# Kernel tuning notes

Measured on AMD Instinct MI355X. Metric: run time of the kernel, lower is better.

The kernel has to match this reference:

```python
import jax, jax.numpy as jnp
import numpy as np

B, T, D, H = 32, 2048, 256, 256  # batch, length, input_size, hidden_size


def _lstm_layer(x, W_ih, W_hh, b, reverse):
    """Single-direction LSTM over time. x: [B,T,Din]; W_ih: [4H,Din]; W_hh: [4H,H]; b: [4H].
    Gate order: i, f, g, o (PyTorch convention). Returns hidden states [B,T,H]."""
    # Precompute input contribution for all timesteps in one big GEMM.
    xg = jnp.einsum('btd,gd->btg', x, W_ih) + b  # [B,T,4H]
    Hh = W_hh.shape[1]
    Bb = x.shape[0]

    def step(carry, xg_t):
        h, c = carry
        g = xg_t + h @ W_hh.T  # [B,4H]
        i, f, gc, o = jnp.split(g, 4, axis=-1)
        c = jax.nn.sigmoid(f) * c + jax.nn.sigmoid(i) * jnp.tanh(gc)
        h = jax.nn.sigmoid(o) * jnp.tanh(c)
        return (h, c), h

    init = (jnp.zeros((Bb, Hh), x.dtype), jnp.zeros((Bb, Hh), x.dtype))
    _, hs = jax.lax.scan(step, init, jnp.swapaxes(xg, 0, 1), reverse=reverse)  # [T,B,H]
    return jnp.swapaxes(hs, 0, 1)  # [B,T,H]


def setup_inputs() -> dict:
    key = jax.random.key(0)
    ks = jax.random.split(key, 13)
    s = 0.05
    G = 4 * H
    inp = {
        'x': jax.random.normal(ks[0], (B, T, D), dtype=jnp.float32),
        # layer 0 (input size D), forward and reverse directions
        'W_ih_f0': jax.random.normal(ks[1], (G, D), dtype=jnp.float32) * s,
        'W_hh_f0': jax.random.normal(ks[2], (G, H), dtype=jnp.float32) * s,
        'b_f0': jnp.zeros((G,), dtype=jnp.float32),
        'W_ih_r0': jax.random.normal(ks[3], (G, D), dtype=jnp.float32) * s,
        'W_hh_r0': jax.random.normal(ks[4], (G, H), dtype=jnp.float32) * s,
        'b_r0': jnp.zeros((G,), dtype=jnp.float32),
        # layer 1 (input size 2H because bidirectional)
        'W_ih_f1': jax.random.normal(ks[5], (G, 2 * H), dtype=jnp.float32) * s,
        'W_hh_f1': jax.random.normal(ks[6], (G, H), dtype=jnp.float32) * s,
        'b_f1': jnp.zeros((G,), dtype=jnp.float32),
        'W_ih_r1': jax.random.normal(ks[7], (G, 2 * H), dtype=jnp.float32) * s,
        'W_hh_r1': jax.random.normal(ks[8], (G, H), dtype=jnp.float32) * s,
        'b_r1': jnp.zeros((G,), dtype=jnp.float32),
    }
    return inp


def reference(x, W_ih_f0, W_hh_f0, b_f0, W_ih_r0, W_hh_r0, b_r0,
              W_ih_f1, W_hh_f1, b_f1, W_ih_r1, W_hh_r1, b_r1):
    # Layer 0: bidirectional over raw input
    h0 = jnp.concatenate([
        _lstm_layer(x, W_ih_f0, W_hh_f0, b_f0, reverse=False),
        _lstm_layer(x, W_ih_r0, W_hh_r0, b_r0, reverse=True),
    ], axis=-1)  # [B,T,2H]
    # Layer 1: bidirectional over concatenated hidden states
    h1 = jnp.concatenate([
        _lstm_layer(h0, W_ih_f1, W_hh_f1, b_f1, reverse=False),
        _lstm_layer(h0, W_ih_r1, W_hh_r1, b_r1, reverse=True),
    ], axis=-1)  # [B,T,2H]
    return h1
```

## Files before the change

### kernel.cpp

```cpp
#include <hip/hip_runtime.h>
#include <stdint.h>


#define Bn 32
#define Tn 2048
#define Hn 256

typedef short short8 __attribute__((ext_vector_type(8)));
typedef float f32x4 __attribute__((ext_vector_type(4)));

__device__ inline unsigned short f2b(float f) {
  union { float f; unsigned u; } v; v.f = f;
  unsigned r = v.u + 0x7fffu + ((v.u >> 16) & 1u);
  return (unsigned short)(r >> 16);
}
__device__ inline float b2f(unsigned short b) {
  union { unsigned u; float f; } v; v.u = ((unsigned)b) << 16;
  return v.f;
}
__device__ inline float sigx(float x) {
  return __builtin_amdgcn_rcpf(1.f + __expf(-x));
}
__device__ inline float tanhx(float x) {
  return 2.f * __builtin_amdgcn_rcpf(1.f + __expf(-2.f * x)) - 1.f;
}

template <int K, bool AF32>
__global__ __launch_bounds__(256, 2) void xg_gemm(
    const void* __restrict__ Ain,
    const float* __restrict__ Wf, const float* __restrict__ bf_,
    const float* __restrict__ Wr, const float* __restrict__ br_,
    unsigned short* __restrict__ xg) {
  constexpr int KI = K / 32;
  const int bid = blockIdx.x;
  const int scan = bid & 1;
  const int sgrp = (bid >> 1) & 7;
  const int mchunk = bid >> 4;
  const int wave = threadIdx.x >> 6;
  const int lane = threadIdx.x & 63;
  const int l15 = lane & 15, quad = lane >> 4;
  const int stripe = sgrp * 4 + wave;
  const int gi0 = stripe * 32;

  const float* W = scan ? Wr : Wf;
  const float* bias = scan ? br_ : bf_;

  short8 bfr[KI][2];
  float bias2[2];
#pragma unroll
  for (int sub = 0; sub < 2; ++sub) {
    const int gi = gi0 + sub * 16 + l15;
    bias2[sub] = bias[gi];
#pragma unroll
    for (int ki = 0; ki < KI; ++ki) {
      const float* src = W + (size_t)gi * K + ki * 32 + quad * 8;
      short8 v;
#pragma unroll
      for (int j = 0; j < 8; ++j) v[j] = (short)f2b(src[j]);
      bfr[ki][sub] = v;
    }
  }

  const size_t scan_off = (size_t)scan << 26;
#pragma unroll 1
  for (int mt0 = 0; mt0 < 16; ++mt0) {
    const int mt = mchunk * 16 + mt0;
    const size_t row = (size_t)mt * 16 + l15;
    f32x4 acc[2];
#pragma unroll
    for (int sub = 0; sub < 2; ++sub) {
      f32x4 bi = {bias2[sub], bias2[sub], bias2[sub], bias2[sub]};
      acc[sub] = bi;
    }
#pragma unroll
    for (int ki = 0; ki < KI; ++ki) {
      short8 af;
      if constexpr (AF32) {
        const float* ap = (const float*)Ain + row * K + ki * 32 + quad * 8;
        f32x4 a0 = *(const f32x4*)ap;
        f32x4 a1 = *(const f32x4*)(ap + 4);
#pragma unroll
        for (int j = 0; j < 4; ++j) { af[j] = (short)f2b(a0[j]); af[4 + j] = (short)f2b(a1[j]); }
      } else {
        const unsigned short* ap = (const unsigned short*)Ain + row * K + ki * 32 + quad * 8;
        af = *(const short8*)ap;
      }
#pragma unroll
      for (int sub = 0; sub < 2; ++sub)
        acc[sub] = __builtin_amdgcn_mfma_f32_16x16x32_bf16(af, bfr[ki][sub], acc[sub], 0, 0, 0);
    }
#pragma unroll
    for (int sub = 0; sub < 2; ++sub) {
      const int gi = gi0 + sub * 16 + l15;
#pragma unroll
      for (int r = 0; r < 4; ++r) {
        const int orow = mt * 16 + quad * 4 + r;
        const int m = orow >> 11, t = orow & 2047;
        xg[scan_off + ((size_t)t * Bn + m) * 1024 + gi] = f2b(acc[sub][r]);
      }
    }
  }
}

template <bool LAYER1>
__global__ __launch_bounds__(256, 1) void lstm_scan(
    const unsigned short* __restrict__ xg,
    const float* __restrict__ Whh_f, const float* __restrict__ Whh_r,
    unsigned short* __restrict__ hbuf,
    int* __restrict__ flags,
    unsigned short* __restrict__ h0out,
    float* __restrict__ dout) {
  const int bid = blockIdx.x;
  const int scan = bid & 1;
  const int wg = bid >> 1;
  const int wave = threadIdx.x >> 6;
  const int lane = threadIdx.x & 63;
  const int slot = wg * 4 + wave;
  const int cg = slot >> 1, mh = slot & 1;
  const int l15 = lane & 15, quad = lane >> 4;
  const int U = cg * 16 + l15;
  const int mrow = mh * 16 + l15;

  const float* Whh = scan ? Whh_r : Whh_f;

  short8 bfh[8][4];
#pragma unroll
  for (int ki = 0; ki < 8; ++ki) {
#pragma unroll
    for (int g = 0; g < 4; ++g) {
      const float* src = Whh + (size_t)(g * Hn + U) * Hn + ki * 32 + quad * 8;
      short8 v;
#pragma unroll
      for (int j = 0; j < 8; ++j) v[j] = (short)f2b(src[j]);
      bfh[ki][g] = v;
    }
  }

  unsigned short* myhb = hbuf + scan * (2 * Bn * Hn);
  int* myflags = flags + scan * 32;
  const size_t scan_off = (size_t)scan << 26;

  float c_st[4] = {0.f, 0.f, 0.f, 0.f};

  for (int s = 0; s < Tn; ++s) {
    const int t = scan ? (Tn - 1 - s) : s;

    const unsigned short* xgp = xg + scan_off + (size_t)t * (Bn * 1024);
    f32x4 acc[4];
#pragma unroll
    for (int g = 0; g < 4; ++g) {
#pragma unroll
      for (int r = 0; r < 4; ++r) {
        const int m = mh * 16 + quad * 4 + r;
        acc[g][r] = b2f(xgp[m * 1024 + g * Hn + U]);
      }
    }

    if (s > 0) {
      for (;;) {
        int v = (lane < 32)
                  ? __hip_atomic_load(&myflags[lane], __ATOMIC_RELAXED, __HIP_MEMORY_SCOPE_AGENT)
                  : s;
        if (__all(v >= s)) break;
        __builtin_amdgcn_s_sleep(1);
      }
      const unsigned long long* hq = (const unsigned long long*)myhb;
      const int pbase = ((s - 1) & 1) * 2048 + mrow * 64;
#pragma unroll
      for (int ki = 0; ki < 8; ++ki) {
        const int idx = pbase + ki * 8 + quad * 2;
        unsigned long long q0 = __hip_atomic_load(hq + idx, __ATOMIC_RELAXED, __HIP_MEMORY_SCOPE_AGENT);
        unsigned long long q1 = __hip_atomic_load(hq + idx + 1, __ATOMIC_RELAXED, __HIP_MEMORY_SCOPE_AGENT);
        union { unsigned long long q[2]; short8 s8; } u;
        u.q[0] = q0; u.q[1] = q1;
#pragma unroll
        for (int g = 0; g < 4; ++g)
          acc[g] = __builtin_amdgcn_mfma_f32_16x16x32_bf16(u.s8, bfh[ki][g], acc[g], 0, 0, 0);
      }
    }

    unsigned int* hw32 = (unsigned int*)(myhb + (s & 1) * (Bn * Hn));
#pragma unroll
    for (int r = 0; r < 4; ++r) {
      const int m = mh * 16 + quad * 4 + r;
      float ig = sigx(acc[0][r]), fg = sigx(acc[1][r]);
      float gg = tanhx(acc[2][r]), og = sigx(acc[3][r]);
      float cv = fg * c_st[r] + ig * gg;
      c_st[r] = cv;
      float hv = og * tanhx(cv);
      unsigned short hb16 = f2b(hv);
      int pk = __shfl_xor((int)hb16, 1);
      if (!(lane & 1)) {
        unsigned int pv = (unsigned)hb16 | ((unsigned)pk << 16);
        __hip_atomic_store(hw32 + m * 128 + (U >> 1), pv, __ATOMIC_RELAXED, __HIP_MEMORY_SCOPE_AGENT);
      }
      if constexpr (!LAYER1) {
        h0out[((size_t)m * Tn + t) * 512 + scan * Hn + U] = hb16;
      } else {
        dout[((size_t)m * Tn + t) * 512 + scan * Hn + U] = hv;
      }
    }

    asm volatile("s_waitcnt vmcnt(0)" ::: "memory");
    if (lane == 0)
      __hip_atomic_store(&myflags[slot], s + 1, __ATOMIC_RELAXED, __HIP_MEMORY_SCOPE_AGENT);
  }
}

extern "C" void kernel_launch(void* const* d_in, const int* in_sizes, int n_in,
                              void* d_out, int out_size, void* d_ws, size_t ws_size,
                              hipStream_t stream) {
  (void)in_sizes; (void)n_in; (void)out_size; (void)ws_size;
  const float* x      = (const float*)d_in[0];
  const float* Wih_f0 = (const float*)d_in[1];
  const float* Whh_f0 = (const float*)d_in[2];
  const float* b_f0   = (const float*)d_in[3];
  const float* Wih_r0 = (const float*)d_in[4];
  const float* Whh_r0 = (const float*)d_in[5];
  const float* b_r0   = (const float*)d_in[6];
  const float* Wih_f1 = (const float*)d_in[7];
  const float* Whh_f1 = (const float*)d_in[8];
  const float* b_f1   = (const float*)d_in[9];
  const float* Wih_r1 = (const float*)d_in[10];
  const float* Whh_r1 = (const float*)d_in[11];
  const float* b_r1   = (const float*)d_in[12];

  char* ws = (char*)d_ws;
  unsigned short* xgbuf = (unsigned short*)ws;
  size_t off = (size_t)2 * Tn * Bn * 1024 * sizeof(unsigned short);
  unsigned short* h0out = (unsigned short*)(ws + off);
  off += (size_t)Bn * Tn * 512 * sizeof(unsigned short);
  unsigned short* hbufA = (unsigned short*)(ws + off); off += 2 * 2 * Bn * Hn * 2;
  unsigned short* hbufB = (unsigned short*)(ws + off); off += 2 * 2 * Bn * Hn * 2;
  int* flagsA = (int*)(ws + off);
  int* flagsB = flagsA + 64;

  hipMemsetAsync(flagsA, 0, 512, stream);

  dim3 blk(256);
  xg_gemm<256, true><<<dim3(4096), blk, 0, stream>>>(
      (const void*)x, Wih_f0, b_f0, Wih_r0, b_r0, xgbuf);
  lstm_scan<false><<<dim3(16), blk, 0, stream>>>(
      xgbuf, Whh_f0, Whh_r0, hbufA, flagsA, h0out, (float*)nullptr);
  xg_gemm<512, false><<<dim3(4096), blk, 0, stream>>>(
      (const void*)h0out, Wih_f1, b_f1, Wih_r1, b_r1, xgbuf);
  lstm_scan<true><<<dim3(16), blk, 0, stream>>>(
      xgbuf, Whh_f1, Whh_r1, hbufB, flagsB, (unsigned short*)nullptr, (float*)d_out);
}
```

Measured before the change: 16.56 ms.

## Run each LSTM scan direction in single workgroups with LDS-based hidden-state exchange

```diff
diff --git a/kernel.cpp b/kernel.cpp
--- a/kernel.cpp
+++ b/kernel.cpp
@@ -8,15 +8,15 @@
 
 typedef short short8 __attribute__((ext_vector_type(8)));
 typedef float f32x4 __attribute__((ext_vector_type(4)));
+typedef unsigned int u32x4 __attribute__((ext_vector_type(4)));
 
 __device__ inline unsigned short f2b(float f) {
   union { float f; unsigned u; } v; v.f = f;
   unsigned r = v.u + 0x7fffu + ((v.u >> 16) & 1u);
   return (unsigned short)(r >> 16);
 }
-__device__ inline float b2f(unsigned short b) {
-  union { unsigned u; float f; } v; v.u = ((unsigned)b) << 16;
-  return v.f;
+__device__ inline float asf(unsigned u) {
+  union { unsigned u; float f; } v; v.u = u; return v.f;
 }
 __device__ inline float sigx(float x) {
   return __builtin_amdgcn_rcpf(1.f + __expf(-x));
@@ -41,6 +41,8 @@
   const int l15 = lane & 15, quad = lane >> 4;
   const int stripe = sgrp * 4 + wave;
   const int gi0 = stripe * 32;
+  const int wp = stripe & 7;
+  const int gg = stripe >> 3;
 
   const float* W = scan ? Wr : Wf;
   const float* bias = scan ? br_ : bf_;
@@ -61,7 +63,7 @@
     }
   }
 
-  const size_t scan_off = (size_t)scan << 26;
+  const size_t scanoff = (size_t)scan << 26;
 #pragma unroll 1
   for (int mt0 = 0; mt0 < 16; ++mt0) {
     const int mt = mchunk * 16 + mt0;
@@ -91,119 +93,153 @@
     }
 #pragma unroll
     for (int sub = 0; sub < 2; ++sub) {
-      const int gi = gi0 + sub * 16 + l15;
 #pragma unroll
       for (int r = 0; r < 4; ++r) {
         const int orow = mt * 16 + quad * 4 + r;
         const int m = orow >> 11, t = orow & 2047;
-        xg[scan_off + ((size_t)t * Bn + m) * 1024 + gi] = f2b(acc[sub][r]);
+        size_t idx = scanoff
+          + ((((size_t)t * 2 + (m >> 4)) * 8 + wp) << 11)
+          + ((size_t)((((m >> 2) & 3) << 4) + l15) << 5)
+          + (sub << 4) + (gg << 2) + (m & 3);
+        xg[idx] = f2b(acc[sub][r]);
       }
     }
   }
 }
 
 template <bool LAYER1>
-__global__ __launch_bounds__(256, 1) void lstm_scan(
+__global__ __launch_bounds__(512, 2) void lstm_scan(
     const unsigned short* __restrict__ xg,
     const float* __restrict__ Whh_f, const float* __restrict__ Whh_r,
-    unsigned short* __restrict__ hbuf,
-    int* __restrict__ flags,
     unsigned short* __restrict__ h0out,
     float* __restrict__ dout) {
+  __shared__ __align__(16) char smem[131072 + 2 * 8448];
+
   const int bid = blockIdx.x;
   const int scan = bid & 1;
-  const int wg = bid >> 1;
+  const int mh = bid >> 1;
   const int wave = threadIdx.x >> 6;
   const int lane = threadIdx.x & 63;
-  const int slot = wg * 4 + wave;
-  const int cg = slot >> 1, mh = slot & 1;
   const int l15 = lane & 15, quad = lane >> 4;
-  const int U = cg * 16 + l15;
-  const int mrow = mh * 16 + l15;
 
   const float* Whh = scan ? Whh_r : Whh_f;
 
-  short8 bfh[8][4];
-#pragma unroll
-  for (int ki = 0; ki < 8; ++ki) {
-#pragma unroll
-    for (int g = 0; g < 4; ++g) {
-      const float* src = Whh + (size_t)(g * Hn + U) * Hn + ki * 32 + quad * 8;
+  short8 wres[2][3][8];
+#pragma unroll
+  for (int uh = 0; uh < 2; ++uh)
+#pragma unroll
+    for (int g = 0; g < 3; ++g)
+#pragma unroll
+      for (int ki = 0; ki < 8; ++ki) {
+        const int col = g * 256 + wave * 32 + uh * 16 + l15;
+        const float* src = Whh + ((size_t)col << 8) + ki * 32 + quad * 8;
+        f32x4 a0 = *(const f32x4*)src;
+        f32x4 a1 = *(const f32x4*)(src + 4);
+        short8 v;
+#pragma unroll
+        for (int j = 0; j < 4; ++j) { v[j] = (short)f2b(a0[j]); v[4 + j] = (short)f2b(a1[j]); }
+        wres[uh][g][ki] = v;
+      }
+#pragma unroll
+  for (int uh = 0; uh < 2; ++uh)
+#pragma unroll
+    for (int ki = 0; ki < 8; ++ki) {
+      const int col = 768 + wave * 32 + uh * 16 + l15;
+      const float* src = Whh + ((size_t)col << 8) + ki * 32 + quad * 8;
+      f32x4 a0 = *(const f32x4*)src;
+      f32x4 a1 = *(const f32x4*)(src + 4);
       short8 v;
 #pragma unroll
-      for (int j = 0; j < 8; ++j) v[j] = (short)f2b(src[j]);
-      bfh[ki][g] = v;
-    }
-  }
-
-  unsigned short* myhb = hbuf + scan * (2 * Bn * Hn);
-  int* myflags = flags + scan * 32;
-  const size_t scan_off = (size_t)scan << 26;
-
-  float c_st[4] = {0.f, 0.f, 0.f, 0.f};
-
+      for (int j = 0; j < 4; ++j) { v[j] = (short)f2b(a0[j]); v[4 + j] = (short)f2b(a1[j]); }
+      *(short8*)(smem + ((((wave << 1) + uh) << 3) + ki) * 1024 + lane * 16) = v;
+    }
+
+  const size_t scanoff = (size_t)scan << 26;
+  const int tstep = scan ? -1 : 1;
+  const int t0 = scan ? (Tn - 1) : 0;
+  const size_t lane_off = (size_t)lane * 32;
+  u32x4 xr[2][2];
+  {
+    const unsigned short* xb =
+        xg + scanoff + ((((size_t)t0 * 2 + mh) * 8 + wave) << 11) + lane_off;
+    xr[0][0] = *(const u32x4*)(xb + 0);
+    xr[0][1] = *(const u32x4*)(xb + 8);
+    xr[1][0] = *(const u32x4*)(xb + 16);
+    xr[1][1] = *(const u32x4*)(xb + 24);
+  }
+
+  char* hbuf = smem + 131072;
+  float c_st[2][4] = {{0.f, 0.f, 0.f, 0.f}, {0.f, 0.f, 0.f, 0.f}};
+
+  __syncthreads();
+
+#pragma unroll 1
   for (int s = 0; s < Tn; ++s) {
     const int t = scan ? (Tn - 1 - s) : s;
-
-    const unsigned short* xgp = xg + scan_off + (size_t)t * (Bn * 1024);
-    f32x4 acc[4];
-#pragma unroll
-    for (int g = 0; g < 4; ++g) {
+    const int tn = (s < Tn - 1) ? (t + tstep) : t;
+    const unsigned short* xbn =
+        xg + scanoff + ((((size_t)tn * 2 + mh) * 8 + wave) << 11) + lane_off;
+    const int p_r = (s - 1) & 1, p_w = s & 1;
+
+#pragma unroll
+    for (int uh = 0; uh < 2; ++uh) {
+      f32x4 acc[4];
+#pragma unroll
+      for (int g = 0; g < 4; ++g) {
+        unsigned lo = xr[uh][g >> 1][2 * (g & 1)];
+        unsigned hi = xr[uh][g >> 1][2 * (g & 1) + 1];
+        acc[g][0] = asf(lo << 16); acc[g][1] = asf(lo & 0xffff0000u);
+        acc[g][2] = asf(hi << 16); acc[g][3] = asf(hi & 0xffff0000u);
+      }
+      if (uh == 1) {
+        xr[0][0] = *(const u32x4*)(xbn + 0);
+        xr[0][1] = *(const u32x4*)(xbn + 8);
+      }
+
+      if (s > 0) {
+        const char* hr = hbuf + p_r * 8448 + l15 * 528 + quad * 16;
+        const char* wl0 = smem + (((wave << 1) + uh) << 13) + lane * 16;
+#pragma unroll
+        for (int ki = 0; ki < 8; ++ki) {
+          short8 a = *(const short8*)(hr + (ki << 6));
+          short8 wl = *(const short8*)(wl0 + (ki << 10));
+          acc[0] = __builtin_amdgcn_mfma_f32_16x16x32_bf16(a, wres[uh][0][ki], acc[0], 0, 0, 0);
+          acc[1] = __builtin_amdgcn_mfma_f32_16x16x32_bf16(a, wres[uh][1][ki], acc[1], 0, 0, 0);
+          acc[2] = __builtin_amdgcn_mfma_f32_16x16x32_bf16(a, wres[uh][2][ki], acc[2], 0, 0, 0);
+          acc[3] = __builtin_amdgcn_mfma_f32_16x16x32_bf16(a, wl,              acc[3], 0, 0, 0);
+        }
+      }
+
+      const int ubase = wave * 32 + uh * 16 + l15;
 #pragma unroll
       for (int r = 0; r < 4; ++r) {
-        const int m = mh * 16 + quad * 4 + r;
-        acc[g][r] = b2f(xgp[m * 1024 + g * Hn + U]);
-      }
-    }
-
-    if (s > 0) {
-      for (;;) {
-        int v = (lane < 32)
-                  ? __hip_atomic_load(&myflags[lane], __ATOMIC_RELAXED, __HIP_MEMORY_SCOPE_AGENT)
-                  : s;
-        if (__all(v >= s)) break;
-        __builtin_amdgcn_s_sleep(1);
-      }
-      const unsigned long long* hq = (const unsigned long long*)myhb;
-      const int pbase = ((s - 1) & 1) * 2048 + mrow * 64;
-#pragma unroll
-      for (int ki = 0; ki < 8; ++ki) {
-        const int idx = pbase + ki * 8 + quad * 2;
-        unsigned long long q0 = __hip_atomic_load(hq + idx, __ATOMIC_RELAXED, __HIP_MEMORY_SCOPE_AGENT);
-        unsigned long long q1 = __hip_atomic_load(hq + idx + 1, __ATOMIC_RELAXED, __HIP_MEMORY_SCOPE_AGENT);
-        union { unsigned long long q[2]; short8 s8; } u;
-        u.q[0] = q0; u.q[1] = q1;
-#pragma unroll
-        for (int g = 0; g < 4; ++g)
-          acc[g] = __builtin_amdgcn_mfma_f32_16x16x32_bf16(u.s8, bfh[ki][g], acc[g], 0, 0, 0);
-      }
-    }
-
-    unsigned int* hw32 = (unsigned int*)(myhb + (s & 1) * (Bn * Hn));
-#pragma unroll
-    for (int r = 0; r < 4; ++r) {
-      const int m = mh * 16 + quad * 4 + r;
-      float ig = sigx(acc[0][r]), fg = sigx(acc[1][r]);
-      float gg = tanhx(acc[2][r]), og = sigx(acc[3][r]);
-      float cv = fg * c_st[r] + ig * gg;
-      c_st[r] = cv;
-      float hv = og * tanhx(cv);
-      unsigned short hb16 = f2b(hv);
-      int pk = __shfl_xor((int)hb16, 1);
-      if (!(lane & 1)) {
-        unsigned int pv = (unsigned)hb16 | ((unsigned)pk << 16);
-        __hip_atomic_store(hw32 + m * 128 + (U >> 1), pv, __ATOMIC_RELAXED, __HIP_MEMORY_SCOPE_AGENT);
-      }
-      if constexpr (!LAYER1) {
-        h0out[((size_t)m * Tn + t) * 512 + scan * Hn + U] = hb16;
-      } else {
-        dout[((size_t)m * Tn + t) * 512 + scan * Hn + U] = hv;
-      }
-    }
-
-    asm volatile("s_waitcnt vmcnt(0)" ::: "memory");
-    if (lane == 0)
-      __hip_atomic_store(&myflags[slot], s + 1, __ATOMIC_RELAXED, __HIP_MEMORY_SCOPE_AGENT);
+        float ig = sigx(acc[0][r]), fg = sigx(acc[1][r]);
+        float gc = tanhx(acc[2][r]), og = sigx(acc[3][r]);
+        float cv = fg * c_st[uh][r] + ig * gc;
+        c_st[uh][r] = cv;
+        float hv = og * tanhx(cv);
+        unsigned short h16 = f2b(hv);
+        int pk = __shfl_xor((int)h16, 1);
+        const int row = quad * 4 + r;
+        if (!(lane & 1)) {
+          unsigned pv = (unsigned)h16 | ((unsigned)pk << 16);
+          *(unsigned*)(hbuf + p_w * 8448 + row * 528 + ubase * 2) = pv;
+        }
+        const int b = mh * 16 + row;
+        if constexpr (!LAYER1) {
+          h0out[(((size_t)b * Tn + t) << 9) + scan * Hn + ubase] = h16;
+        } else {
+          dout[(((size_t)b * Tn + t) << 9) + scan * Hn + ubase] = hv;
+        }
+      }
+
+      if (uh == 1) {
+        xr[1][0] = *(const u32x4*)(xbn + 16);
+        xr[1][1] = *(const u32x4*)(xbn + 24);
+      }
+    }
+
+    __syncthreads();
   }
 }
 
@@ -229,21 +265,14 @@
   unsigned short* xgbuf = (unsigned short*)ws;
   size_t off = (size_t)2 * Tn * Bn * 1024 * sizeof(unsigned short);
   unsigned short* h0out = (unsigned short*)(ws + off);
-  off += (size_t)Bn * Tn * 512 * sizeof(unsigned short);
-  unsigned short* hbufA = (unsigned short*)(ws + off); off += 2 * 2 * Bn * Hn * 2;
-  unsigned short* hbufB = (unsigned short*)(ws + off); off += 2 * 2 * Bn * Hn * 2;
-  int* flagsA = (int*)(ws + off);
-  int* flagsB = flagsA + 64;
-
-  hipMemsetAsync(flagsA, 0, 512, stream);
-
-  dim3 blk(256);
-  xg_gemm<256, true><<<dim3(4096), blk, 0, stream>>>(
+
+  dim3 blkA(256), blkB(512);
+  xg_gemm<256, true><<<dim3(4096), blkA, 0, stream>>>(
       (const void*)x, Wih_f0, b_f0, Wih_r0, b_r0, xgbuf);
-  lstm_scan<false><<<dim3(16), blk, 0, stream>>>(
-      xgbuf, Whh_f0, Whh_r0, hbufA, flagsA, h0out, (float*)nullptr);
-  xg_gemm<512, false><<<dim3(4096), blk, 0, stream>>>(
+  lstm_scan<false><<<dim3(4), blkB, 0, stream>>>(
+      xgbuf, Whh_f0, Whh_r0, h0out, (float*)nullptr);
+  xg_gemm<512, false><<<dim3(4096), blkA, 0, stream>>>(
       (const void*)h0out, Wih_f1, b_f1, Wih_r1, b_r1, xgbuf);
-  lstm_scan<true><<<dim3(16), blk, 0, stream>>>(
-      xgbuf, Whh_f1, Whh_r1, hbufB, flagsB, (unsigned short*)nullptr, (float*)d_out);
-}
+  lstm_scan<true><<<dim3(4), blkB, 0, stream>>>(
+      xgbuf, Whh_f1, Whh_r1, (unsigned short*)nullptr, (float*)d_out);
+}
```

Result: faster. 14.15 ms (-14.6%).
